# Kernel optimization log

Hardware: AMD Instinct MI355X
Metric: run time of the kernel (lower is better)

Reference implementation:

```python
import jax, jax.numpy as jnp
import numpy as np

B = 4; N_LIG = 150; N_PROT = 550; N = 700
H = 128; HEADS = 4; KPH = 32; HPH = 32
L = 6; K = 48; EDGE_CH = 128; CUTOFF = 10.0
PROT_F = 27; NUM_CLASSES = 13
LOG2 = 0.6931471805599453
FLAT = N * H  # 89600, matches fc1 in_features


def ssp(x):
    # ShiftedSoftplus
    return jax.nn.softplus(x) - LOG2


def lin(x, w, b):
    # torch Linear convention: w is [out, in]
    return jnp.einsum('...i,oi->...o', x, w) + b


def setup_inputs() -> dict:
    key = jax.random.key(0)
    ki = iter(jax.random.split(key, 40))

    def nrm(shape, fan_in):
        return jax.random.normal(next(ki), shape, jnp.float32) / np.sqrt(fan_in).astype(np.float32)

    lig_pos = jax.random.normal(next(ki), (B, N_LIG, 3), jnp.float32) * 3.0
    lig_t = jax.random.randint(next(ki), (B, N_LIG, 1), 0, NUM_CLASSES).astype(jnp.float32)
    state = jnp.concatenate([lig_pos, lig_t], axis=-1)  # [B, N_LIG, 4]
    protein_pos_v = jnp.concatenate([
        jax.random.normal(next(ki), (B, N_PROT, 3), jnp.float32) * 3.0,
        jax.random.normal(next(ki), (B, N_PROT, PROT_F), jnp.float32)], axis=-1)  # [B, N_PROT, 30]

    inp = dict(state=state, protein_pos_v=protein_pos_v)
    inp['w_prot'] = nrm((H, PROT_F), PROT_F); inp['b_prot'] = jnp.zeros((H,), jnp.float32)
    inp['w_lig'] = nrm((H, NUM_CLASSES), NUM_CLASSES); inp['b_lig'] = jnp.zeros((H,), jnp.float32)
    # per-layer stacked encoder params (grouped 1x1 conv == per-head linear, no bias)
    inp['wq'] = nrm((L, HEADS, KPH, HPH), HPH)
    inp['wk'] = nrm((L, HEADS, KPH, HPH), HPH)
    inp['wv'] = nrm((L, HEADS, HPH, HPH), HPH)
    inp['wkn1_w'] = nrm((L, KPH, EDGE_CH), EDGE_CH); inp['wkn1_b'] = jnp.zeros((L, KPH), jnp.float32)
    inp['wkn2_w'] = nrm((L, KPH, KPH), KPH); inp['wkn2_b'] = jnp.zeros((L, KPH), jnp.float32)
    inp['wkl_w'] = nrm((L, KPH, KPH), KPH); inp['wkl_b'] = jnp.zeros((L, KPH), jnp.float32)
    inp['wvn1_w'] = nrm((L, HPH, EDGE_CH), EDGE_CH); inp['wvn1_b'] = jnp.zeros((L, HPH), jnp.float32)
    inp['wvn2_w'] = nrm((L, HPH, HPH), HPH); inp['wvn2_b'] = jnp.zeros((L, HPH), jnp.float32)
    inp['wvl_w'] = nrm((L, HPH, HPH), HPH); inp['wvl_b'] = jnp.zeros((L, HPH), jnp.float32)
    inp['cen_w'] = nrm((L, H, H), H); inp['cen_b'] = jnp.zeros((L, H), jnp.float32)
    inp['out_w'] = nrm((L, H, H), H); inp['out_b'] = jnp.zeros((L, H), jnp.float32)
    inp['ln_g'] = jnp.ones((L, H), jnp.float32); inp['ln_b'] = jnp.zeros((L, H), jnp.float32)
    inp['fc1_w'] = nrm((128, FLAT), FLAT); inp['fc1_b'] = jnp.zeros((128,), jnp.float32)
    inp['fc2_w'] = nrm((64, 128), 128); inp['fc2_b'] = jnp.zeros((64,), jnp.float32)
    inp['fc3_w'] = nrm((1, 64), 64); inp['fc3_b'] = jnp.zeros((1,), jnp.float32)
    return inp


def reference(state, protein_pos_v, w_prot, b_prot, w_lig, b_lig, wq, wk, wv,
              wkn1_w, wkn1_b, wkn2_w, wkn2_b, wkl_w, wkl_b,
              wvn1_w, wvn1_b, wvn2_w, wvn2_b, wvl_w, wvl_b,
              cen_w, cen_b, out_w, out_b, ln_g, ln_b,
              fc1_w, fc1_b, fc2_w, fc2_b, fc3_w, fc3_b):
    lig_pos = state[..., :3]
    lig_t = jax.lax.stop_gradient(state[..., 3]).astype(jnp.int32)
    lig_oh = jax.nn.one_hot(lig_t, NUM_CLASSES, dtype=jnp.float32)
    prot_pos = protein_pos_v[..., :3]
    prot_v = protein_pos_v[..., 3:]
    # compose_context: stable sort by batch -> protein atoms then ligand atoms per complex
    h = jnp.concatenate([lin(prot_v, w_prot, b_prot), lin(lig_oh, w_lig, b_lig)], axis=1)  # [B,N,H]
    pos = jnp.concatenate([prot_pos, lig_pos], axis=1)  # [B,N,3]
    # kNN graph (k nearest neighbors, no self loops), batched per complex
    d2 = jnp.sum((pos[:, :, None, :] - pos[:, None, :, :]) ** 2, axis=-1)  # [B,N,N]
    d2 = d2 + jnp.eye(N, dtype=d2.dtype) * 1e9
    _, nbr = jax.lax.top_k(-d2, K)  # [B,N,K]
    dist = jnp.sqrt(jnp.take_along_axis(d2, nbr, axis=2))  # [B,N,K]
    # Gaussian smearing of edge lengths
    offset = jnp.linspace(0.0, CUTOFF, EDGE_CH)
    coeff = -0.5 / (offset[1] - offset[0]) ** 2
    edge_attr = jnp.exp(coeff * (dist[..., None] - offset) ** 2)  # [B,N,K,E]
    gat = jax.vmap(lambda a, i: a[i])  # per-batch neighbor gather
    for l in range(L):
        xh = h.reshape(B, N, HEADS, HPH)
        q = jnp.einsum('bnhd,hkd->bnhk', xh, wq[l])
        kx = jnp.einsum('bnhd,hkd->bnhk', xh, wk[l])
        vx = jnp.einsum('bnhd,hkd->bnhk', xh, wv[l])
        w_k = lin(ssp(lin(edge_attr, wkn1_w[l], wkn1_b[l])), wkn2_w[l], wkn2_b[l])  # [B,N,K,KPH]
        keys_j = lin(w_k[:, :, :, None, :] * gat(kx, nbr), wkl_w[l], wkl_b[l])  # [B,N,K,heads,KPH]
        qk = jnp.einsum('bnhk,bnmhk->bnmh', q, keys_j)  # per-edge attention logits
        alpha = jax.nn.softmax(qk, axis=2)  # scatter_softmax over each node's K edges
        w_v = lin(ssp(lin(edge_attr, wvn1_w[l], wvn1_b[l])), wvn2_w[l], wvn2_b[l])  # [B,N,K,HPH]
        msg = lin(w_v[:, :, :, None, :] * gat(vx, nbr), wvl_w[l], wvl_b[l])  # [B,N,K,heads,HPH]
        aggr = jnp.einsum('bnmh,bnmhd->bnhd', alpha, msg).reshape(B, N, H)
        x = lin(h, cen_w[l], cen_b[l]) + aggr
        mu = jnp.mean(x, axis=-1, keepdims=True)
        var = jnp.var(x, axis=-1, keepdims=True)
        x = (x - mu) / jnp.sqrt(var + 1e-5) * ln_g[l] + ln_b[l]
        h = h + lin(ssp(x), out_w[l], out_b[l])  # residual per interaction block
    # decoup_batch + pad_tensor: constant 700 nodes/complex -> plain reshape
    x = h.reshape(B, FLAT)
    x = jax.nn.relu(lin(x, fc1_w, fc1_b))
    x = jax.nn.relu(lin(x, fc2_w, fc2_b))
    return lin(x, fc3_w, fc3_b)  # [B,1]
```

## Files before the change

### kernel.cpp

```cpp
#include <hip/hip_runtime.h>
#include <hip/hip_fp16.h>
#include <math.h>

constexpr int cB   = 4;
constexpr int cNL  = 150;
constexpr int cNP  = 550;
constexpr int cN   = 700;
constexpr int cH   = 128;
constexpr int cHeads = 4;
constexpr int cL   = 6;
constexpr int cK   = 48;
constexpr int cPF  = 27;
constexpr int cNC  = 13;
constexpr int cFLAT = cN * cH;
constexpr int cEdges = cB * cN * cK;

constexpr int   TABN = 4096;
#define TAB_DMAX 11.0f
#define TAB_HT   (TAB_DMAX / (float)(TABN - 1))
#define TAB_INV  ((float)(TABN - 1) / TAB_DMAX)

#define RBF_STEP (10.0f / 127.0f)
#define RBF_COEFF (-0.5f / (RBF_STEP * RBF_STEP))
#define LOG2F_C 0.69314718055994530942f

__device__ __forceinline__ float sspf(float x) {
    float ax = fabsf(x);
    return fmaxf(x, 0.0f) + __logf(1.0f + __expf(-ax)) - LOG2F_C;
}

__device__ __forceinline__ int mbcnt64(unsigned long long m) {
    return __builtin_amdgcn_mbcnt_hi((unsigned)(m >> 32),
           __builtin_amdgcn_mbcnt_lo((unsigned)m, 0));
}

__global__ void __launch_bounds__(256) k_init(
    const float* __restrict__ wq, const float* __restrict__ wk, const float* __restrict__ wv,
    const float* __restrict__ wkn1_w, const float* __restrict__ wvn1_w,
    const float* __restrict__ wkn2_w, const float* __restrict__ wvn2_w,
    const float* __restrict__ wvl_w,
    const float* __restrict__ cen_w, const float* __restrict__ out_w,
    float* __restrict__ wqT, float* __restrict__ wkT, float* __restrict__ wvT,
    float* __restrict__ w1Tk, float* __restrict__ w1Tv,
    float* __restrict__ w2Tk, float* __restrict__ w2Tv,
    float* __restrict__ wvlT,
    float* __restrict__ cenT, float* __restrict__ outT,
    const float* __restrict__ state, const float* __restrict__ ppv,
    const float* __restrict__ w_prot, const float* __restrict__ b_prot,
    const float* __restrict__ w_lig, const float* __restrict__ b_lig,
    float* __restrict__ h, float* __restrict__ pos)
{
    if (blockIdx.x < 1320) {
        int idx = blockIdx.x * 256 + threadIdx.x;
        if (idx < 3 * 24576) {
            int seg = idx / 24576, i = idx % 24576;
            const float* src = seg == 0 ? wq : (seg == 1 ? wk : wv);
            float* dst = seg == 0 ? wqT : (seg == 1 ? wkT : wvT);
            int l = i / 4096, r = i % 4096;
            int hh = r / 1024, r2 = r % 1024;
            int d = r2 / 32, k = r2 % 32;
            dst[i] = src[(((size_t)l * 4 + hh) * 32 + k) * 32 + d];
            return;
        }
        idx -= 3 * 24576;
        if (idx < 2 * 24576) {
            int seg = idx / 24576, i = idx % 24576;
            const float* src = seg == 0 ? wkn1_w : wvn1_w;
            float* dst = seg == 0 ? w1Tk : w1Tv;
            int l = i / 4096, r = i % 4096;
            int c = r / 32, o = r % 32;
            dst[i] = src[((size_t)l * 32 + o) * 128 + c];
            return;
        }
        idx -= 2 * 24576;
        if (idx < 3 * 6144) {
            int seg = idx / 6144, i = idx % 6144;
            const float* src = seg == 0 ? wkn2_w : (seg == 1 ? wvn2_w : wvl_w);
            float* dst = seg == 0 ? w2Tk : (seg == 1 ? w2Tv : wvlT);
            int l = i / 1024, r = i % 1024;
            int c = r / 32, o = r % 32;
            dst[i] = src[((size_t)l * 32 + o) * 32 + c];
            return;
        }
        idx -= 3 * 6144;
        int seg = idx / 98304, i = idx % 98304;
        const float* src = seg == 0 ? cen_w : out_w;
        float* dst = seg == 0 ? cenT : outT;
        int l = i / 16384, r = i % 16384;
        int ii = r / 128, o = r % 128;
        dst[i] = src[((size_t)l * 128 + o) * 128 + ii];
        return;
    }
    int rel = blockIdx.x - 1320;
    int node = rel * 2 + (threadIdx.x >> 7);
    int b = node / cN, n = node % cN;
    int o = threadIdx.x & 127;
    int lane = threadIdx.x & 63;
    float out;
    if (n < cNP) {
        const float* src = ppv + ((size_t)b * cNP + n) * 30;
        float v = (lane < 30) ? src[lane] : 0.f;
        float s = b_prot[o];
        #pragma unroll
        for (int f = 0; f < cPF; f++) s += w_prot[o * cPF + f] * __shfl(v, 3 + f);
        out = s;
        if (o < 3) pos[((size_t)b * cN + n) * 3 + o] = v;
    } else {
        int nl = n - cNP;
        const float* src = state + ((size_t)b * cNL + nl) * 4;
        float v = (lane < 4) ? src[lane] : 0.f;
        int t = (int)__shfl(v, 3);
        out = w_lig[o * cNC + t] + b_lig[o];
        if (o < 3) pos[((size_t)b * cN + n) * 3 + o] = v;
    }
    h[((size_t)b * cN + n) * cH + o] = out;
}

__global__ void __launch_bounds__(256) k_knn(
    const float* __restrict__ pos, int* __restrict__ nbr, float* __restrict__ dist,
    const float* __restrict__ w1Tk, const float* __restrict__ wkn1_b,
    const float* __restrict__ w2Tk, const float* __restrict__ wkn2_b,
    const float* __restrict__ w1Tv, const float* __restrict__ wvn1_b,
    const float* __restrict__ w2Tv, const float* __restrict__ wvn2_b,
    float* __restrict__ tab,
    const float* __restrict__ hbuf,
    const float* __restrict__ wqT, const float* __restrict__ wkT, const float* __restrict__ wvT,
    float* __restrict__ q0, __half* __restrict__ kx0, __half* __restrict__ vx0)
{
    int tid = threadIdx.x;
    if (blockIdx.x < cN) {
        int lane = tid & 63;
        int node = blockIdx.x * 4 + (tid >> 6);
        int b = node / cN, n = node % cN;
        const float* pb = pos + (size_t)b * cN * 3;
        float px = pb[n * 3 + 0], py = pb[n * 3 + 1], pz = pb[n * 3 + 2];
        float d2v[11];
        #pragma unroll
        for (int s = 0; s < 11; s++) {
            int j = lane + s * 64;
            float d2 = 1e30f;
            if (j < cN) {
                float dx = pb[j * 3 + 0] - px;
                float dy = pb[j * 3 + 1] - py;
                float dz = pb[j * 3 + 2] - pz;
                d2 = dx * dx + dy * dy + dz * dz;
                if (j == n) d2 = 1e9f;
            }
            d2v[s] = d2;
        }
        unsigned p = 0;
        for (int bit = 30; bit >= 0; --bit) {
            unsigned t = p | (1u << bit);
            int cnt = 0;
            #pragma unroll
            for (int s = 0; s < 11; s++)
                cnt += __popcll(__ballot(__float_as_uint(d2v[s]) < t));
            if (cnt <= 47) p = t;
        }
        int c_lt = 0;
        #pragma unroll
        for (int s = 0; s < 11; s++)
            c_lt += __popcll(__ballot(__float_as_uint(d2v[s]) < p));
        int base = 0, ebase = c_lt, need = 48 - c_lt;
        #pragma unroll
        for (int s = 0; s < 11; s++) {
            unsigned u = __float_as_uint(d2v[s]);
            unsigned long long blt = __ballot(u < p);
            unsigned long long beq = __ballot(u == p);
            int posn = -1;
            int bl = mbcnt64(blt);
            if (u < p) posn = base + bl;
            base += __popcll(blt);
            int r = mbcnt64(beq);
            int cs = __popcll(beq);
            int take = need < cs ? need : cs;
            if (u == p && r < take) posn = ebase + r;
            ebase += take; need -= take;
            if (posn >= 0) {
                nbr[(size_t)node * cK + posn] = s * 64 + lane;
                dist[(size_t)node * cK + posn] = sqrtf(d2v[s]);
            }
        }
        return;
    }
    if (blockIdx.x < cN + TABN / 4) {
        int rel = blockIdx.x - cN;
        int lane = tid & 63;
        int e = rel * 4 + (tid >> 6);
        int side = lane >> 5, o = lane & 31;
        float d = (float)e * TAB_HT;
        float z = d * (127.0f / 10.0f);
        int c0 = (int)floorf(z) - 7;
        c0 = c0 < 0 ? 0 : (c0 > 112 ? 112 : c0);
        int i = lane & 15;
        float tt = d - RBF_STEP * (float)(c0 + i);
        float eav = __expf(RBF_COEFF * tt * tt);
        const float* w1T = (side ? w1Tv : w1Tk);
        const float* b1  = (side ? wvn1_b : wkn1_b);
        const float* w2T = (side ? w2Tv : w2Tk);
        const float* b2  = (side ? wvn2_b : wkn2_b);
        int srcb = side * 32;
        for (int l = 0; l < cL; l++) {
            float s = b1[l * 32 + o];
            const float* w1p = w1T + (size_t)l * 4096;
            #pragma unroll
            for (int ii = 0; ii < 16; ii++)
                s += w1p[(c0 + ii) * 32 + o] * __shfl(eav, ii);
            float t1 = sspf(s);
            float s2 = b2[l * 32 + o];
            const float* w2p = w2T + (size_t)l * 1024;
            #pragma unroll
            for (int cc = 0; cc < 32; cc++)
                s2 += w2p[cc * 32 + o] * __shfl(t1, srcb + cc);
            tab[((size_t)(l * TABN + e) * 2 + side) * 32 + o] = s2;
        }
        return;
    }
    int bn = (blockIdx.x - cN - TABN / 4) * 2 + (tid >> 7);
    int o = tid & 127;
    int hh = o >> 5, kq = o & 31;
    float hval = hbuf[(size_t)bn * cH + o];
    size_t wo = ((size_t)0 * 4 + hh) * 1024;
    const float* bq = wqT + wo;
    const float* bk = wkT + wo;
    const float* bv = wvT + wo;
    int srcb = (hh & 1) * 32;
    float sq = 0.f, sk = 0.f, sv = 0.f;
    #pragma unroll
    for (int d = 0; d < 32; d++) {
        float x = __shfl(hval, srcb + d);
        sq += bq[d * 32 + kq] * x;
        sk += bk[d * 32 + kq] * x;
        sv += bv[d * 32 + kq] * x;
    }
    q0[(size_t)bn * cH + o] = sq;
    kx0[(size_t)bn * cH + o] = __float2half(sk);
    vx0[(size_t)bn * cH + o] = __float2half(sv);
}

__global__ void __launch_bounds__(256) k_attn(
    int l,
    const float* __restrict__ h_in, const float* __restrict__ qr,
    const __half* __restrict__ kxr, const __half* __restrict__ vxr,
    const int* __restrict__ nbr, const float* __restrict__ dist,
    const float* __restrict__ tab,
    const float* __restrict__ wkl_w,
    const float* __restrict__ wvlT, const float* __restrict__ wvl_b,
    const float* __restrict__ cenT, const float* __restrict__ cen_b,
    const float* __restrict__ outT, const float* __restrict__ out_b,
    const float* __restrict__ ln_g, const float* __restrict__ ln_b,
    float* __restrict__ h_out,
    float* __restrict__ qw, __half* __restrict__ kxw, __half* __restrict__ vxw,
    const float* __restrict__ wqT, const float* __restrict__ wkT, const float* __restrict__ wvT)
{
    int tid = threadIdx.x;
    int u = tid >> 7;
    int o = tid & 127;
    int bn = blockIdx.x;
    int b = bn / cN;
    int hh = o >> 5, c = o & 31;
    int srcb = (hh & 1) * 32;

    __shared__ float sh_h[cH];
    __shared__ float sh_t[cH];
    __shared__ float sh_p[2][cH];
    __shared__ float sh_c[2][cH];
    __shared__ float sh_qk[cK * cHeads];
    __shared__ int   sh_nb[cK];
    __shared__ int   sh_idx[cK];
    __shared__ float sh_frac[cK];
    __shared__ float red[4][2];

    float qv = qr[(size_t)bn * cH + o];
    if (u == 0) sh_h[o] = h_in[(size_t)bn * cH + o];
    if (u == 1 && o < cK) {
        sh_nb[o] = nbr[(size_t)bn * cK + o];
        float d = dist[(size_t)bn * cK + o];
        float z = d * TAB_INV;
        int idx = (int)z;
        if (idx > TABN - 2) idx = TABN - 2;
        sh_idx[o] = idx;
        sh_frac[o] = fminf(z - (float)idx, 1.0f);
    }
    __syncthreads();

    const float* wklp = wkl_w + l * 1024;
    float qt = 0.f;
    #pragma unroll 8
    for (int k = 0; k < 32; k++) qt += __shfl(qv, srcb + k) * wklp[k * 32 + c];

    const __half* kxb = kxr + (size_t)b * cN * cH;
    const __half* vxb = vxr + (size_t)b * cN * cH;
    const float* tabl = tab + (size_t)l * TABN * 64;
    int mbase = u * (cK / 2);

    #pragma unroll 4
    for (int mi = 0; mi < cK / 2; mi += 2) {
        int m = mbase + mi;
        int j0 = sh_nb[m], j1 = sh_nb[m + 1];
        float k0 = __half2float(kxb[(size_t)j0 * cH + o]);
        float k1 = __half2float(kxb[(size_t)j1 * cH + o]);
        const float* t0 = tabl + (size_t)sh_idx[m] * 64 + c;
        const float* t1p = tabl + (size_t)sh_idx[m + 1] * 64 + c;
        float w0 = t0[0] + sh_frac[m] * (t0[64] - t0[0]);
        float w1 = t1p[0] + sh_frac[m + 1] * (t1p[64] - t1p[0]);
        float pa = qt * w0 * k0;
        float pb = qt * w1 * k1;
        float x = (c & 1) ? pb : pa;
        float y = (c & 1) ? pa : pb;
        x += __shfl_xor(y, 1);
        x += __shfl_xor(x, 2);
        x += __shfl_xor(x, 4);
        x += __shfl_xor(x, 8);
        x += __shfl_xor(x, 16);
        if (c < 2) sh_qk[(m + c) * cHeads + hh] = x;
    }
    __syncthreads();

    if (u == 0) {
        float v1 = sh_qk[c * cHeads + hh];
        float v2 = (c < cK - 32) ? sh_qk[(32 + c) * cHeads + hh] : -1e30f;
        float mx = fmaxf(v1, v2);
        #pragma unroll
        for (int off = 16; off; off >>= 1) mx = fmaxf(mx, __shfl_xor(mx, off));
        float e1 = __expf(v1 - mx);
        float e2 = (c < cK - 32) ? __expf(v2 - mx) : 0.f;
        float s = e1 + e2;
        #pragma unroll
        for (int off = 16; off; off >>= 1) s += __shfl_xor(s, off);
        float inv = 1.0f / s;
        sh_qk[c * cHeads + hh] = e1 * inv;
        if (c < cK - 32) sh_qk[(32 + c) * cHeads + hh] = e2 * inv;
    }
    __syncthreads();

    float t0a = 0.f, t1a = 0.f;
    #pragma unroll 4
    for (int mi = 0; mi < cK / 2; mi += 2) {
        int m = mbase + mi;
        int j0 = sh_nb[m], j1 = sh_nb[m + 1];
        const float* tv0 = tabl + (size_t)sh_idx[m] * 64 + 32 + c;
        const float* tv1 = tabl + (size_t)sh_idx[m + 1] * 64 + 32 + c;
        float w0 = tv0[0] + sh_frac[m] * (tv0[64] - tv0[0]);
        float w1 = tv1[0] + sh_frac[m + 1] * (tv1[64] - tv1[0]);
        t0a += sh_qk[m * cHeads + hh] * (w0 * __half2float(vxb[(size_t)j0 * cH + o]));
        t1a += sh_qk[(m + 1) * cHeads + hh] * (w1 * __half2float(vxb[(size_t)j1 * cH + o]));
    }
    sh_p[u][o] = t0a + t1a;
    __syncthreads();

    const float* wvlTp = wvlT + l * 1024;
    float xpart = 0.f;
    #pragma unroll
    for (int i = u * 16; i < u * 16 + 16; i++)
        xpart += wvlTp[i * 32 + c] * (sh_p[0][hh * 32 + i] + sh_p[1][hh * 32 + i]);
    if (u == 0) xpart += wvl_b[l * 32 + c] + cen_b[l * cH + o];

    const float* cenTp = cenT + (size_t)l * cH * cH;
    {
        float x0 = 0.f, x1 = 0.f;
        #pragma unroll 4
        for (int i = u * 64; i < u * 64 + 64; i += 2) {
            x0 += cenTp[i * cH + o] * sh_h[i];
            x1 += cenTp[(i + 1) * cH + o] * sh_h[i + 1];
        }
        xpart += x0 + x1;
    }
    sh_c[u][o] = xpart;
    __syncthreads();
    float x = sh_c[0][o] + sh_c[1][o];

    float s1 = x, s2 = x * x;
    #pragma unroll
    for (int off = 32; off; off >>= 1) {
        s1 += __shfl_xor(s1, off);
        s2 += __shfl_xor(s2, off);
    }
    int wid = tid >> 6;
    if ((tid & 63) == 0) { red[wid][0] = s1; red[wid][1] = s2; }
    __syncthreads();
    float tot1 = red[0][0] + red[1][0], tot2 = red[0][1] + red[1][1];
    float mu = tot1 * (1.0f / 128.0f);
    float var = tot2 * (1.0f / 128.0f) - mu * mu;
    float xn = (x - mu) * rsqrtf(var + 1e-5f);
    xn = xn * ln_g[l * cH + o] + ln_b[l * cH + o];
    float sx = sspf(xn);
    if (u == 0) sh_t[o] = sx;
    __syncthreads();

    const float* outTp = outT + (size_t)l * cH * cH;
    {
        float o0 = 0.f, o1 = 0.f;
        #pragma unroll 4
        for (int i = u * 64; i < u * 64 + 64; i += 2) {
            o0 += outTp[i * cH + o] * sh_t[i];
            o1 += outTp[(i + 1) * cH + o] * sh_t[i + 1];
        }
        sh_c[u][o] = o0 + o1;
    }
    __syncthreads();
    float hnew = sh_h[o] + out_b[l * cH + o] + sh_c[0][o] + sh_c[1][o];
    if (u == 0) h_out[(size_t)bn * cH + o] = hnew;

    if (l < cL - 1) {
        size_t wo = ((size_t)(l + 1) * 4 + hh) * 1024;
        if (u == 0) {
            const float* bq = wqT + wo;
            float sq = 0.f;
            #pragma unroll
            for (int d = 0; d < 32; d++) sq += bq[d * 32 + c] * __shfl(hnew, srcb + d);
            qw[(size_t)bn * cH + o] = sq;
        } else {
            const float* bk = wkT + wo;
            const float* bv = wvT + wo;
            float sk = 0.f, sv = 0.f;
            #pragma unroll
            for (int d = 0; d < 32; d++) {
                float xv = __shfl(hnew, srcb + d);
                sk += bk[d * 32 + c] * xv;
                sv += bv[d * 32 + c] * xv;
            }
            kxw[(size_t)bn * cH + o] = __float2half(sk);
            vxw[(size_t)bn * cH + o] = __float2half(sv);
        }
    }
}

__global__ void __launch_bounds__(256) k_fc1p(const float* __restrict__ hbuf,
                                              const float* __restrict__ w,
                                              float* __restrict__ partial)
{
    int o = blockIdx.x >> 2, qp = blockIdx.x & 3;
    int tid = threadIdx.x;
    constexpr int CH = cFLAT / 4;
    const float4* wr = (const float4*)(w + (size_t)o * cFLAT + qp * CH);
    float a[4] = {0.f, 0.f, 0.f, 0.f};
    for (int i = tid; i < CH / 4; i += 256) {
        float4 wv = wr[i];
        #pragma unroll
        for (int bb = 0; bb < 4; bb++) {
            float4 hv = ((const float4*)(hbuf + (size_t)bb * cFLAT + qp * CH))[i];
            a[bb] += wv.x * hv.x + wv.y * hv.y + wv.z * hv.z + wv.w * hv.w;
        }
    }
    #pragma unroll
    for (int off = 32; off; off >>= 1) {
        #pragma unroll
        for (int bb = 0; bb < 4; bb++) a[bb] += __shfl_xor(a[bb], off);
    }
    __shared__ float red[4][4];
    if ((tid & 63) == 0) {
        #pragma unroll
        for (int bb = 0; bb < 4; bb++) red[tid >> 6][bb] = a[bb];
    }
    __syncthreads();
    if (tid < 4) {
        float s = red[0][tid] + red[1][tid] + red[2][tid] + red[3][tid];
        partial[((size_t)o * 4 + qp) * 4 + tid] = s;
    }
}

__global__ void __launch_bounds__(512) k_head2(const float* __restrict__ partial,
                                               const float* __restrict__ fc1_b,
                                               const float* __restrict__ fc2_w,
                                               const float* __restrict__ fc2_b,
                                               const float* __restrict__ fc3_w,
                                               const float* __restrict__ fc3_b,
                                               float* __restrict__ out)
{
    int tid = threadIdx.x;
    __shared__ float y1[4][128];
    __shared__ float y2[4][64];
    {
        int bb = tid >> 7, o = tid & 127;
        float s = fc1_b[o];
        #pragma unroll
        for (int qp = 0; qp < 4; qp++) s += partial[((size_t)o * 4 + qp) * 4 + bb];
        y1[bb][o] = fmaxf(s, 0.f);
    }
    __syncthreads();
    if (tid < 256) {
        int bb = tid >> 6, o = tid & 63;
        float s = fc2_b[o];
        #pragma unroll 8
        for (int i = 0; i < 128; i++) s += fc2_w[o * 128 + i] * y1[bb][i];
        y2[bb][o] = fmaxf(s, 0.f);
    }
    __syncthreads();
    if (tid < 4) {
        float s = fc3_b[0];
        #pragma unroll 8
        for (int i = 0; i < 64; i++) s += fc3_w[i] * y2[tid][i];
        out[tid] = s;
    }
}

extern "C" void kernel_launch(void* const* d_in, const int* in_sizes, int n_in,
                              void* d_out, int out_size, void* d_ws, size_t ws_size,
                              hipStream_t stream) {
    const float* state  = (const float*)d_in[0];
    const float* ppv    = (const float*)d_in[1];
    const float* w_prot = (const float*)d_in[2];
    const float* b_prot = (const float*)d_in[3];
    const float* w_lig  = (const float*)d_in[4];
    const float* b_lig  = (const float*)d_in[5];
    const float* wq     = (const float*)d_in[6];
    const float* wk     = (const float*)d_in[7];
    const float* wv     = (const float*)d_in[8];
    const float* wkn1_w = (const float*)d_in[9];
    const float* wkn1_b = (const float*)d_in[10];
    const float* wkn2_w = (const float*)d_in[11];
    const float* wkn2_b = (const float*)d_in[12];
    const float* wkl_w  = (const float*)d_in[13];
    const float* wvn1_w = (const float*)d_in[15];
    const float* wvn1_b = (const float*)d_in[16];
    const float* wvn2_w = (const float*)d_in[17];
    const float* wvn2_b = (const float*)d_in[18];
    const float* wvl_w  = (const float*)d_in[19];
    const float* wvl_b  = (const float*)d_in[20];
    const float* cen_w  = (const float*)d_in[21];
    const float* cen_b  = (const float*)d_in[22];
    const float* out_w  = (const float*)d_in[23];
    const float* out_b  = (const float*)d_in[24];
    const float* ln_g   = (const float*)d_in[25];
    const float* ln_b   = (const float*)d_in[26];
    const float* fc1_w  = (const float*)d_in[27];
    const float* fc1_b  = (const float*)d_in[28];
    const float* fc2_w  = (const float*)d_in[29];
    const float* fc2_b  = (const float*)d_in[30];
    const float* fc3_w  = (const float*)d_in[31];
    const float* fc3_b  = (const float*)d_in[32];

    float* ws = (float*)d_ws;
    size_t off = 0;
    float* pos   = ws + off; off += (size_t)cB * cN * 3;
    float* h_a   = ws + off; off += (size_t)cB * cN * cH;
    float* h_b   = ws + off; off += (size_t)cB * cN * cH;
    float* qA    = ws + off; off += (size_t)cB * cN * cH;
    float* qB    = ws + off; off += (size_t)cB * cN * cH;
    __half* kA   = (__half*)(ws + off); off += (size_t)cB * cN * cH / 2;
    __half* vA   = (__half*)(ws + off); off += (size_t)cB * cN * cH / 2;
    __half* kB   = (__half*)(ws + off); off += (size_t)cB * cN * cH / 2;
    __half* vB   = (__half*)(ws + off); off += (size_t)cB * cN * cH / 2;
    float* distb = ws + off; off += (size_t)cEdges;
    int*   nbrb  = (int*)(ws + off); off += (size_t)cEdges;
    float* tabb  = ws + off; off += (size_t)cL * TABN * 64;
    float* wqT   = ws + off; off += 24576;
    float* wkT   = ws + off; off += 24576;
    float* wvT   = ws + off; off += 24576;
    float* w1Tk  = ws + off; off += 24576;
    float* w1Tv  = ws + off; off += 24576;
    float* w2Tk  = ws + off; off += 6144;
    float* w2Tv  = ws + off; off += 6144;
    float* wvlT  = ws + off; off += 6144;
    float* cenT  = ws + off; off += 98304;
    float* outT  = ws + off; off += 98304;
    float* partial = ws + off; off += 2048;

    k_init<<<2720, 256, 0, stream>>>(wq, wk, wv, wkn1_w, wvn1_w, wkn2_w, wvn2_w,
                                     wvl_w, cen_w, out_w,
                                     wqT, wkT, wvT, w1Tk, w1Tv, w2Tk, w2Tv, wvlT, cenT, outT,
                                     state, ppv, w_prot, b_prot, w_lig, b_lig, h_a, pos);
    k_knn<<<cN + TABN / 4 + cB * cN / 2, 256, 0, stream>>>(
        pos, nbrb, distb,
        w1Tk, wkn1_b, w2Tk, wkn2_b, w1Tv, wvn1_b, w2Tv, wvn2_b, tabb,
        h_a, wqT, wkT, wvT, qA, kA, vA);

    float* hc = h_a;
    float* hn = h_b;
    for (int l = 0; l < cL; l++) {
        float* qr = (l & 1) ? qB : qA;
        __half* kr = (l & 1) ? kB : kA;
        __half* vr = (l & 1) ? vB : vA;
        float* qw2 = (l & 1) ? qA : qB;
        __half* kw2 = (l & 1) ? kA : kB;
        __half* vw2 = (l & 1) ? vA : vB;
        k_attn<<<cB * cN, 256, 0, stream>>>(l, hc, qr, kr, vr, nbrb, distb, tabb,
            wkl_w, wvlT, wvl_b, cenT, cen_b, outT, out_b, ln_g, ln_b,
            hn, qw2, kw2, vw2, wqT, wkT, wvT);
        float* tmp = hc; hc = hn; hn = tmp;
    }

    k_fc1p<<<512, 256, 0, stream>>>(hc, fc1_w, partial);
    k_head2<<<1, 512, 0, stream>>>(partial, fc1_b, fc2_w, fc2_b, fc3_w, fc3_b, (float*)d_out);
}
```

Measured before the change: 324.0 us.

## Repack weights for float4 loads, pair table entries, and halve attention block size

Weights are repacked at init into a k-interleaved layout so each thread can load float4 vectors in the q/k/v, wkl, wvl, cen and out matvecs. The RBF lookup table now stores each entry next to its successor, so interpolation takes a single float2 load instead of two scattered loads, at the cost of doubling the table's memory. The attention kernel drops from 256 to 128 threads per node, which removes the two-half split of edges and matvec rows and the shared-memory partial reductions and syncs. In exchange each thread does twice the serial work, and there may be less latency hiding per block.

After: 408.5 us. +26.1%, slower.

```diff
diff --git a/kernel.cpp b/kernel.cpp
--- a/kernel.cpp
+++ b/kernel.cpp
@@ -38,28 +38,26 @@
     const float* __restrict__ wq, const float* __restrict__ wk, const float* __restrict__ wv,
     const float* __restrict__ wkn1_w, const float* __restrict__ wvn1_w,
     const float* __restrict__ wkn2_w, const float* __restrict__ wvn2_w,
-    const float* __restrict__ wvl_w,
+    const float* __restrict__ wkl_w, const float* __restrict__ wvl_w,
     const float* __restrict__ cen_w, const float* __restrict__ out_w,
-    float* __restrict__ wqT, float* __restrict__ wkT, float* __restrict__ wvT,
+    float* __restrict__ wqP, float* __restrict__ wkP, float* __restrict__ wvP,
     float* __restrict__ w1Tk, float* __restrict__ w1Tv,
     float* __restrict__ w2Tk, float* __restrict__ w2Tv,
-    float* __restrict__ wvlT,
-    float* __restrict__ cenT, float* __restrict__ outT,
+    float* __restrict__ wklP, float* __restrict__ wvlP,
+    float* __restrict__ cenP, float* __restrict__ outP,
     const float* __restrict__ state, const float* __restrict__ ppv,
     const float* __restrict__ w_prot, const float* __restrict__ b_prot,
     const float* __restrict__ w_lig, const float* __restrict__ b_lig,
     float* __restrict__ h, float* __restrict__ pos)
 {
-    if (blockIdx.x < 1320) {
+    if (blockIdx.x < 1344) {
         int idx = blockIdx.x * 256 + threadIdx.x;
         if (idx < 3 * 24576) {
             int seg = idx / 24576, i = idx % 24576;
             const float* src = seg == 0 ? wq : (seg == 1 ? wk : wv);
-            float* dst = seg == 0 ? wqT : (seg == 1 ? wkT : wvT);
-            int l = i / 4096, r = i % 4096;
-            int hh = r / 1024, r2 = r % 1024;
-            int d = r2 / 32, k = r2 % 32;
-            dst[i] = src[(((size_t)l * 4 + hh) * 32 + k) * 32 + d];
+            float* dst = seg == 0 ? wqP : (seg == 1 ? wkP : wvP);
+            int j = i & 3, k = (i >> 2) & 31, d4 = (i >> 7) & 7, hl = i >> 10;
+            dst[i] = src[((size_t)hl * 32 + k) * 32 + 4 * d4 + j];
             return;
         }
         idx -= 3 * 24576;
@@ -73,25 +71,40 @@
             return;
         }
         idx -= 2 * 24576;
-        if (idx < 3 * 6144) {
+        if (idx < 2 * 6144) {
             int seg = idx / 6144, i = idx % 6144;
-            const float* src = seg == 0 ? wkn2_w : (seg == 1 ? wvn2_w : wvl_w);
-            float* dst = seg == 0 ? w2Tk : (seg == 1 ? w2Tv : wvlT);
+            const float* src = seg == 0 ? wkn2_w : wvn2_w;
+            float* dst = seg == 0 ? w2Tk : w2Tv;
             int l = i / 1024, r = i % 1024;
             int c = r / 32, o = r % 32;
             dst[i] = src[((size_t)l * 32 + o) * 32 + c];
             return;
         }
-        idx -= 3 * 6144;
-        int seg = idx / 98304, i = idx % 98304;
-        const float* src = seg == 0 ? cen_w : out_w;
-        float* dst = seg == 0 ? cenT : outT;
-        int l = i / 16384, r = i % 16384;
-        int ii = r / 128, o = r % 128;
-        dst[i] = src[((size_t)l * 128 + o) * 128 + ii];
+        idx -= 2 * 6144;
+        if (idx < 6144) {
+            int i = idx;
+            int j = i & 3, c = (i >> 2) & 31, k4 = (i >> 7) & 7, l = i >> 10;
+            wklP[i] = wkl_w[(size_t)l * 1024 + (4 * k4 + j) * 32 + c];
+            return;
+        }
+        idx -= 6144;
+        if (idx < 6144) {
+            int i = idx;
+            int j = i & 3, c = (i >> 2) & 31, i4 = (i >> 7) & 7, l = i >> 10;
+            wvlP[i] = wvl_w[((size_t)l * 32 + c) * 32 + 4 * i4 + j];
+            return;
+        }
+        idx -= 6144;
+        {
+            int seg = idx / 98304, i = idx % 98304;
+            const float* src = seg == 0 ? cen_w : out_w;
+            float* dst = seg == 0 ? cenP : outP;
+            int j = i & 3, o = (i >> 2) & 127, i4 = (i >> 9) & 31, l = i >> 14;
+            dst[i] = src[((size_t)l * 128 + o) * 128 + 4 * i4 + j];
+        }
         return;
     }
-    int rel = blockIdx.x - 1320;
+    int rel = blockIdx.x - 1344;
     int node = rel * 2 + (threadIdx.x >> 7);
     int b = node / cN, n = node % cN;
     int o = threadIdx.x & 127;
@@ -122,9 +135,9 @@
     const float* __restrict__ w2Tk, const float* __restrict__ wkn2_b,
     const float* __restrict__ w1Tv, const float* __restrict__ wvn1_b,
     const float* __restrict__ w2Tv, const float* __restrict__ wvn2_b,
-    float* __restrict__ tab,
+    float* __restrict__ tabP,
     const float* __restrict__ hbuf,
-    const float* __restrict__ wqT, const float* __restrict__ wkT, const float* __restrict__ wvT,
+    const float* __restrict__ wqP, const float* __restrict__ wkP, const float* __restrict__ wvP,
     float* __restrict__ q0, __half* __restrict__ kx0, __half* __restrict__ vx0)
 {
     int tid = threadIdx.x;
@@ -212,7 +225,9 @@
             #pragma unroll
             for (int cc = 0; cc < 32; cc++)
                 s2 += w2p[cc * 32 + o] * __shfl(t1, srcb + cc);
-            tab[((size_t)(l * TABN + e) * 2 + side) * 32 + o] = s2;
+            tabP[((((size_t)l * TABN + e) * 2 + side) * 32 + o) * 2] = s2;
+            if (e > 0)
+                tabP[((((size_t)l * TABN + (e - 1)) * 2 + side) * 32 + o) * 2 + 1] = s2;
         }
         return;
     }
@@ -220,60 +235,59 @@
     int o = tid & 127;
     int hh = o >> 5, kq = o & 31;
     float hval = hbuf[(size_t)bn * cH + o];
-    size_t wo = ((size_t)0 * 4 + hh) * 1024;
-    const float* bq = wqT + wo;
-    const float* bk = wkT + wo;
-    const float* bv = wvT + wo;
     int srcb = (hh & 1) * 32;
+    const float4* bq4 = (const float4*)wqP + (size_t)hh * 256 + kq;
+    const float4* bk4 = (const float4*)wkP + (size_t)hh * 256 + kq;
+    const float4* bv4 = (const float4*)wvP + (size_t)hh * 256 + kq;
     float sq = 0.f, sk = 0.f, sv = 0.f;
     #pragma unroll
-    for (int d = 0; d < 32; d++) {
-        float x = __shfl(hval, srcb + d);
-        sq += bq[d * 32 + kq] * x;
-        sk += bk[d * 32 + kq] * x;
-        sv += bv[d * 32 + kq] * x;
+    for (int d4 = 0; d4 < 8; d4++) {
+        float4 a = bq4[d4 * 32], b4 = bk4[d4 * 32], v4 = bv4[d4 * 32];
+        float x0 = __shfl(hval, srcb + 4 * d4 + 0);
+        float x1 = __shfl(hval, srcb + 4 * d4 + 1);
+        float x2 = __shfl(hval, srcb + 4 * d4 + 2);
+        float x3 = __shfl(hval, srcb + 4 * d4 + 3);
+        sq += a.x * x0 + a.y * x1 + a.z * x2 + a.w * x3;
+        sk += b4.x * x0 + b4.y * x1 + b4.z * x2 + b4.w * x3;
+        sv += v4.x * x0 + v4.y * x1 + v4.z * x2 + v4.w * x3;
     }
     q0[(size_t)bn * cH + o] = sq;
     kx0[(size_t)bn * cH + o] = __float2half(sk);
     vx0[(size_t)bn * cH + o] = __float2half(sv);
 }
 
-__global__ void __launch_bounds__(256) k_attn(
+__global__ void __launch_bounds__(128) k_attn(
     int l,
     const float* __restrict__ h_in, const float* __restrict__ qr,
     const __half* __restrict__ kxr, const __half* __restrict__ vxr,
     const int* __restrict__ nbr, const float* __restrict__ dist,
-    const float* __restrict__ tab,
-    const float* __restrict__ wkl_w,
-    const float* __restrict__ wvlT, const float* __restrict__ wvl_b,
-    const float* __restrict__ cenT, const float* __restrict__ cen_b,
-    const float* __restrict__ outT, const float* __restrict__ out_b,
+    const float* __restrict__ tabP,
+    const float* __restrict__ wklP,
+    const float* __restrict__ wvlP, const float* __restrict__ wvl_b,
+    const float* __restrict__ cenP, const float* __restrict__ cen_b,
+    const float* __restrict__ outP, const float* __restrict__ out_b,
     const float* __restrict__ ln_g, const float* __restrict__ ln_b,
     float* __restrict__ h_out,
     float* __restrict__ qw, __half* __restrict__ kxw, __half* __restrict__ vxw,
-    const float* __restrict__ wqT, const float* __restrict__ wkT, const float* __restrict__ wvT)
+    const float* __restrict__ wqP, const float* __restrict__ wkP, const float* __restrict__ wvP)
 {
-    int tid = threadIdx.x;
-    int u = tid >> 7;
-    int o = tid & 127;
+    int o = threadIdx.x;
     int bn = blockIdx.x;
     int b = bn / cN;
     int hh = o >> 5, c = o & 31;
     int srcb = (hh & 1) * 32;
 
-    __shared__ float sh_h[cH];
-    __shared__ float sh_t[cH];
-    __shared__ float sh_p[2][cH];
-    __shared__ float sh_c[2][cH];
+    __shared__ __align__(16) float sh_h[cH];
+    __shared__ __align__(16) float sh_t[cH];
     __shared__ float sh_qk[cK * cHeads];
     __shared__ int   sh_nb[cK];
     __shared__ int   sh_idx[cK];
     __shared__ float sh_frac[cK];
-    __shared__ float red[4][2];
-
+    __shared__ float red[2][2];
+
+    sh_h[o] = h_in[(size_t)bn * cH + o];
     float qv = qr[(size_t)bn * cH + o];
-    if (u == 0) sh_h[o] = h_in[(size_t)bn * cH + o];
-    if (u == 1 && o < cK) {
+    if (o < cK) {
         sh_nb[o] = nbr[(size_t)bn * cK + o];
         float d = dist[(size_t)bn * cK + o];
         float z = d * TAB_INV;
@@ -284,26 +298,30 @@
     }
     __syncthreads();
 
-    const float* wklp = wkl_w + l * 1024;
+    const float4* wklp4 = (const float4*)wklP + (size_t)l * 256 + c;
     float qt = 0.f;
-    #pragma unroll 8
-    for (int k = 0; k < 32; k++) qt += __shfl(qv, srcb + k) * wklp[k * 32 + c];
+    #pragma unroll
+    for (int k4 = 0; k4 < 8; k4++) {
+        float4 w4 = wklp4[k4 * 32];
+        qt += w4.x * __shfl(qv, srcb + 4 * k4 + 0)
+            + w4.y * __shfl(qv, srcb + 4 * k4 + 1)
+            + w4.z * __shfl(qv, srcb + 4 * k4 + 2)
+            + w4.w * __shfl(qv, srcb + 4 * k4 + 3);
+    }
 
     const __half* kxb = kxr + (size_t)b * cN * cH;
     const __half* vxb = vxr + (size_t)b * cN * cH;
-    const float* tabl = tab + (size_t)l * TABN * 64;
-    int mbase = u * (cK / 2);
+    const float2* tab2 = (const float2*)tabP + (size_t)l * TABN * 64;
 
     #pragma unroll 4
-    for (int mi = 0; mi < cK / 2; mi += 2) {
-        int m = mbase + mi;
+    for (int m = 0; m < cK; m += 2) {
         int j0 = sh_nb[m], j1 = sh_nb[m + 1];
         float k0 = __half2float(kxb[(size_t)j0 * cH + o]);
         float k1 = __half2float(kxb[(size_t)j1 * cH + o]);
-        const float* t0 = tabl + (size_t)sh_idx[m] * 64 + c;
-        const float* t1p = tabl + (size_t)sh_idx[m + 1] * 64 + c;
-        float w0 = t0[0] + sh_frac[m] * (t0[64] - t0[0]);
-        float w1 = t1p[0] + sh_frac[m + 1] * (t1p[64] - t1p[0]);
+        float2 t0 = tab2[((size_t)sh_idx[m] * 2 + 0) * 32 + c];
+        float2 t1 = tab2[((size_t)sh_idx[m + 1] * 2 + 0) * 32 + c];
+        float w0 = t0.x + sh_frac[m] * (t0.y - t0.x);
+        float w1 = t1.x + sh_frac[m + 1] * (t1.y - t1.x);
         float pa = qt * w0 * k0;
         float pb = qt * w1 * k1;
         float x = (c & 1) ? pb : pa;
@@ -317,7 +335,7 @@
     }
     __syncthreads();
 
-    if (u == 0) {
+    {
         float v1 = sh_qk[c * cHeads + hh];
         float v2 = (c < cK - 32) ? sh_qk[(32 + c) * cHeads + hh] : -1e30f;
         float mx = fmaxf(v1, v2);
@@ -336,39 +354,41 @@
 
     float t0a = 0.f, t1a = 0.f;
     #pragma unroll 4
-    for (int mi = 0; mi < cK / 2; mi += 2) {
-        int m = mbase + mi;
+    for (int m = 0; m < cK; m += 2) {
         int j0 = sh_nb[m], j1 = sh_nb[m + 1];
-        const float* tv0 = tabl + (size_t)sh_idx[m] * 64 + 32 + c;
-        const float* tv1 = tabl + (size_t)sh_idx[m + 1] * 64 + 32 + c;
-        float w0 = tv0[0] + sh_frac[m] * (tv0[64] - tv0[0]);
-        float w1 = tv1[0] + sh_frac[m + 1] * (tv1[64] - tv1[0]);
-        t0a += sh_qk[m * cHeads + hh] * (w0 * __half2float(vxb[(size_t)j0 * cH + o]));
-        t1a += sh_qk[(m + 1) * cHeads + hh] * (w1 * __half2float(vxb[(size_t)j1 * cH + o]));
-    }
-    sh_p[u][o] = t0a + t1a;
-    __syncthreads();
-
-    const float* wvlTp = wvlT + l * 1024;
-    float xpart = 0.f;
+        float v0 = __half2float(vxb[(size_t)j0 * cH + o]);
+        float v1 = __half2float(vxb[(size_t)j1 * cH + o]);
+        float2 s0 = tab2[((size_t)sh_idx[m] * 2 + 1) * 32 + c];
+        float2 s1 = tab2[((size_t)sh_idx[m + 1] * 2 + 1) * 32 + c];
+        float w0 = s0.x + sh_frac[m] * (s0.y - s0.x);
+        float w1 = s1.x + sh_frac[m + 1] * (s1.y - s1.x);
+        t0a += sh_qk[m * cHeads + hh] * (w0 * v0);
+        t1a += sh_qk[(m + 1) * cHeads + hh] * (w1 * v1);
+    }
+    sh_t[o] = t0a + t1a;
+    __syncthreads();
+
+    const float4* wvlp4 = (const float4*)wvlP + (size_t)l * 256 + c;
+    const float4* st4 = (const float4*)&sh_t[hh * 32];
+    float aggr = wvl_b[l * 32 + c];
     #pragma unroll
-    for (int i = u * 16; i < u * 16 + 16; i++)
-        xpart += wvlTp[i * 32 + c] * (sh_p[0][hh * 32 + i] + sh_p[1][hh * 32 + i]);
-    if (u == 0) xpart += wvl_b[l * 32 + c] + cen_b[l * cH + o];
-
-    const float* cenTp = cenT + (size_t)l * cH * cH;
-    {
-        float x0 = 0.f, x1 = 0.f;
-        #pragma unroll 4
-        for (int i = u * 64; i < u * 64 + 64; i += 2) {
-            x0 += cenTp[i * cH + o] * sh_h[i];
-            x1 += cenTp[(i + 1) * cH + o] * sh_h[i + 1];
-        }
-        xpart += x0 + x1;
-    }
-    sh_c[u][o] = xpart;
-    __syncthreads();
-    float x = sh_c[0][o] + sh_c[1][o];
+    for (int i4 = 0; i4 < 8; i4++) {
+        float4 w4 = wvlp4[i4 * 32];
+        float4 t4 = st4[i4];
+        aggr += w4.x * t4.x + w4.y * t4.y + w4.z * t4.z + w4.w * t4.w;
+    }
+
+    const float4* cenp4 = (const float4*)cenP + (size_t)l * 4096 + o;
+    const float4* sh4 = (const float4*)sh_h;
+    float xa = 0.f, xb = 0.f;
+    #pragma unroll 4
+    for (int i4 = 0; i4 < 32; i4 += 2) {
+        float4 wa = cenp4[i4 * 128], wb = cenp4[(i4 + 1) * 128];
+        float4 ha = sh4[i4], hb = sh4[i4 + 1];
+        xa += wa.x * ha.x + wa.y * ha.y + wa.z * ha.z + wa.w * ha.w;
+        xb += wb.x * hb.x + wb.y * hb.y + wb.z * hb.z + wb.w * hb.w;
+    }
+    float x = cen_b[l * cH + o] + aggr + xa + xb;
 
     float s1 = x, s2 = x * x;
     #pragma unroll
@@ -376,8 +396,8 @@
         s1 += __shfl_xor(s1, off);
         s2 += __shfl_xor(s2, off);
     }
-    int wid = tid >> 6;
-    if ((tid & 63) == 0) { red[wid][0] = s1; red[wid][1] = s2; }
+    int wid = o >> 6;
+    if ((o & 63) == 0) { red[wid][0] = s1; red[wid][1] = s2; }
     __syncthreads();
     float tot1 = red[0][0] + red[1][0], tot2 = red[0][1] + red[1][1];
     float mu = tot1 * (1.0f / 128.0f);
@@ -385,44 +405,42 @@
     float xn = (x - mu) * rsqrtf(var + 1e-5f);
     xn = xn * ln_g[l * cH + o] + ln_b[l * cH + o];
     float sx = sspf(xn);
-    if (u == 0) sh_t[o] = sx;
-    __syncthreads();
-
-    const float* outTp = outT + (size_t)l * cH * cH;
-    {
-        float o0 = 0.f, o1 = 0.f;
-        #pragma unroll 4
-        for (int i = u * 64; i < u * 64 + 64; i += 2) {
-            o0 += outTp[i * cH + o] * sh_t[i];
-            o1 += outTp[(i + 1) * cH + o] * sh_t[i + 1];
-        }
-        sh_c[u][o] = o0 + o1;
-    }
-    __syncthreads();
-    float hnew = sh_h[o] + out_b[l * cH + o] + sh_c[0][o] + sh_c[1][o];
-    if (u == 0) h_out[(size_t)bn * cH + o] = hnew;
+    sh_t[o] = sx;
+    __syncthreads();
+
+    const float4* outp4 = (const float4*)outP + (size_t)l * 4096 + o;
+    const float4* st4b = (const float4*)sh_t;
+    float oa = 0.f, ob = 0.f;
+    #pragma unroll 4
+    for (int i4 = 0; i4 < 32; i4 += 2) {
+        float4 wa = outp4[i4 * 128], wb = outp4[(i4 + 1) * 128];
+        float4 ta = st4b[i4], tb = st4b[i4 + 1];
+        oa += wa.x * ta.x + wa.y * ta.y + wa.z * ta.z + wa.w * ta.w;
+        ob += wb.x * tb.x + wb.y * tb.y + wb.z * tb.z + wb.w * tb.w;
+    }
+    float hnew = sh_h[o] + out_b[l * cH + o] + oa + ob;
+    h_out[(size_t)bn * cH + o] = hnew;
 
     if (l < cL - 1) {
-        size_t wo = ((size_t)(l + 1) * 4 + hh) * 1024;
-        if (u == 0) {
-            const float* bq = wqT + wo;
-            float sq = 0.f;
-            #pragma unroll
-            for (int d = 0; d < 32; d++) sq += bq[d * 32 + c] * __shfl(hnew, srcb + d);
-            qw[(size_t)bn * cH + o] = sq;
-        } else {
-            const float* bk = wkT + wo;
-            const float* bv = wvT + wo;
-            float sk = 0.f, sv = 0.f;
-            #pragma unroll
-            for (int d = 0; d < 32; d++) {
-                float xv = __shfl(hnew, srcb + d);
-                sk += bk[d * 32 + c] * xv;
-                sv += bv[d * 32 + c] * xv;
-            }
-            kxw[(size_t)bn * cH + o] = __float2half(sk);
-            vxw[(size_t)bn * cH + o] = __float2half(sv);
-        }
+        size_t wo = ((size_t)(l + 1) * 4 + hh) * 256 + c;
+        const float4* bq4 = (const float4*)wqP + wo;
+        const float4* bk4 = (const float4*)wkP + wo;
+        const float4* bv4 = (const float4*)wvP + wo;
+        float sq = 0.f, sk = 0.f, sv = 0.f;
+        #pragma unroll
+        for (int d4 = 0; d4 < 8; d4++) {
+            float4 a = bq4[d4 * 32], b4 = bk4[d4 * 32], v4 = bv4[d4 * 32];
+            float x0 = __shfl(hnew, srcb + 4 * d4 + 0);
+            float x1 = __shfl(hnew, srcb + 4 * d4 + 1);
+            float x2 = __shfl(hnew, srcb + 4 * d4 + 2);
+            float x3 = __shfl(hnew, srcb + 4 * d4 + 3);
+            sq += a.x * x0 + a.y * x1 + a.z * x2 + a.w * x3;
+            sk += b4.x * x0 + b4.y * x1 + b4.z * x2 + b4.w * x3;
+            sv += v4.x * x0 + v4.y * x1 + v4.z * x2 + v4.w * x3;
+        }
+        qw[(size_t)bn * cH + o] = sq;
+        kxw[(size_t)bn * cH + o] = __float2half(sk);
+        vxw[(size_t)bn * cH + o] = __float2half(sv);
     }
 }
 
@@ -544,27 +562,28 @@
     __half* vB   = (__half*)(ws + off); off += (size_t)cB * cN * cH / 2;
     float* distb = ws + off; off += (size_t)cEdges;
     int*   nbrb  = (int*)(ws + off); off += (size_t)cEdges;
-    float* tabb  = ws + off; off += (size_t)cL * TABN * 64;
-    float* wqT   = ws + off; off += 24576;
-    float* wkT   = ws + off; off += 24576;
-    float* wvT   = ws + off; off += 24576;
+    float* tabb  = ws + off; off += (size_t)cL * TABN * 64 * 2;
+    float* wqP   = ws + off; off += 24576;
+    float* wkP   = ws + off; off += 24576;
+    float* wvP   = ws + off; off += 24576;
     float* w1Tk  = ws + off; off += 24576;
     float* w1Tv  = ws + off; off += 24576;
     float* w2Tk  = ws + off; off += 6144;
     float* w2Tv  = ws + off; off += 6144;
-    float* wvlT  = ws + off; off += 6144;
-    float* cenT  = ws + off; off += 98304;
-    float* outT  = ws + off; off += 98304;
+    float* wklP  = ws + off; off += 6144;
+    float* wvlP  = ws + off; off += 6144;
+    float* cenP  = ws + off; off += 98304;
+    float* outP  = ws + off; off += 98304;
     float* partial = ws + off; off += 2048;
 
-    k_init<<<2720, 256, 0, stream>>>(wq, wk, wv, wkn1_w, wvn1_w, wkn2_w, wvn2_w,
-                                     wvl_w, cen_w, out_w,
-                                     wqT, wkT, wvT, w1Tk, w1Tv, w2Tk, w2Tv, wvlT, cenT, outT,
-                                     state, ppv, w_prot, b_prot, w_lig, b_lig, h_a, pos);
+    k_init<<<1344 + cB * cN / 2, 256, 0, stream>>>(
+        wq, wk, wv, wkn1_w, wvn1_w, wkn2_w, wvn2_w, wkl_w, wvl_w, cen_w, out_w,
+        wqP, wkP, wvP, w1Tk, w1Tv, w2Tk, w2Tv, wklP, wvlP, cenP, outP,
+        state, ppv, w_prot, b_prot, w_lig, b_lig, h_a, pos);
     k_knn<<<cN + TABN / 4 + cB * cN / 2, 256, 0, stream>>>(
         pos, nbrb, distb,
         w1Tk, wkn1_b, w2Tk, wkn2_b, w1Tv, wvn1_b, w2Tv, wvn2_b, tabb,
-        h_a, wqT, wkT, wvT, qA, kA, vA);
+        h_a, wqP, wkP, wvP, qA, kA, vA);
 
     float* hc = h_a;
     float* hn = h_b;
@@ -575,9 +594,9 @@
         float* qw2 = (l & 1) ? qA : qB;
         __half* kw2 = (l & 1) ? kA : kB;
         __half* vw2 = (l & 1) ? vA : vB;
-        k_attn<<<cB * cN, 256, 0, stream>>>(l, hc, qr, kr, vr, nbrb, distb, tabb,
-            wkl_w, wvlT, wvl_b, cenT, cen_b, outT, out_b, ln_g, ln_b,
-            hn, qw2, kw2, vw2, wqT, wkT, wvT);
+        k_attn<<<cB * cN, 128, 0, stream>>>(l, hc, qr, kr, vr, nbrb, distb, tabb,
+            wklP, wvlP, wvl_b, cenP, cen_b, outP, out_b, ln_g, ln_b,
+            hn, qw2, kw2, vw2, wqP, wkP, wvP);
         float* tmp = hc; hc = hn; hn = tmp;
     }
 
```
